# Optimization experiments

Hardware: AMD Instinct MI355X
Metric: run time of the kernel (lower is better)

Reference implementation:

```python
import jax, jax.numpy as jnp
import numpy as np

EPS = 1e-5

def cal_pcm(cen, s):
    # circ_shift in the original is exactly a circular roll of the HxW plane.
    r = lambda dy, dx: jnp.roll(cen, (dy, dx), axis=(2, 3))
    s1 = (r(-s, -s) - cen) * (r(s, s) - cen)   # NW/SE diagonal pair
    s2 = (r(-s, 0) - cen) * (r(s, 0) - cen)    # N/S pair
    s3 = (r(-s, s) - cen) * (r(s, -s) - cen)   # NE/SW diagonal pair
    s4 = (r(0, s) - cen) * (r(0, -s) - cen)    # E/W pair
    return jnp.minimum(jnp.minimum(s1, s2), jnp.minimum(s3, s4))

def batchnorm(x, gamma, beta):
    # training-mode BN: batch statistics over (N,H,W)
    mean = x.mean(axis=(0, 2, 3), keepdims=True)
    var = x.var(axis=(0, 2, 3), keepdims=True)
    xn = (x - mean) * jax.lax.rsqrt(var + EPS)
    return xn * gamma[None, :, None, None] + beta[None, :, None, None]

def se_att(x, w1, b1, g1, be1, w2, b2, g2, be2):
    # AdaptiveAvgPool2d(1) -> 1x1 conv -> BN -> ReLU -> 1x1 conv -> BN -> Sigmoid
    p = x.mean(axis=(2, 3), keepdims=True)                      # [B,C,1,1]
    y = jnp.einsum('oc,bcij->boij', w1, p) + b1[None, :, None, None]
    y = jax.nn.relu(batchnorm(y, g1, be1))
    y = jnp.einsum('oc,bcij->boij', w2, y) + b2[None, :, None, None]
    return jax.nn.sigmoid(batchnorm(y, g2, be2))

def setup_inputs() -> dict:
    key = jax.random.key(0)
    ks = jax.random.split(key, 8)
    B, C, H, W = 4, 64, 384, 384
    IC = C // 2
    inp = {
        'cen': jax.random.normal(ks[0], (B, C, H, W), dtype=jnp.float32),
        'bn1_g': jnp.ones((C,), jnp.float32), 'bn1_b': jnp.zeros((C,), jnp.float32),
        'bn2_g': jnp.ones((C,), jnp.float32), 'bn2_b': jnp.zeros((C,), jnp.float32),
        'td_w1': jax.random.normal(ks[1], (IC, C), jnp.float32) * 0.1,
        'td_b1': jnp.zeros((IC,), jnp.float32),
        'td_g1': jnp.ones((IC,), jnp.float32), 'td_be1': jnp.zeros((IC,), jnp.float32),
        'td_w2': jax.random.normal(ks[2], (C, IC), jnp.float32) * 0.1,
        'td_b2': jnp.zeros((C,), jnp.float32),
        'td_g2': jnp.ones((C,), jnp.float32), 'td_be2': jnp.zeros((C,), jnp.float32),
        'bu_w1': jax.random.normal(ks[3], (IC, C), jnp.float32) * 0.1,
        'bu_b1': jnp.zeros((IC,), jnp.float32),
        'bu_g1': jnp.ones((IC,), jnp.float32), 'bu_be1': jnp.zeros((IC,), jnp.float32),
        'bu_w2': jax.random.normal(ks[4], (C, IC), jnp.float32) * 0.1,
        'bu_b2': jnp.zeros((C,), jnp.float32),
        'bu_g2': jnp.ones((C,), jnp.float32), 'bu_be2': jnp.zeros((C,), jnp.float32),
    }
    return inp

def reference(cen, bn1_g, bn1_b, bn2_g, bn2_b,
              td_w1, td_b1, td_g1, td_be1, td_w2, td_b2, td_g2, td_be2,
              bu_w1, bu_b1, bu_g1, bu_be1, bu_w2, bu_b2, bu_g2, bu_be2):
    pcm13 = batchnorm(cal_pcm(cen, 13), bn1_g, bn1_b)
    pcm17 = batchnorm(cal_pcm(cen, 17), bn2_g, bn2_b)
    topdown_wei = se_att(pcm17, td_w1, td_b1, td_g1, td_be1, td_w2, td_b2, td_g2, td_be2)
    bottomup_wei = se_att(pcm13, bu_w1, bu_b1, bu_g1, bu_be1, bu_w2, bu_b2, bu_g2, bu_be2)
    return topdown_wei * pcm13 + bottomup_wei * pcm17
```

## Files before the change

### kernel.cpp

```cpp
#include <hip/hip_runtime.h>
#include <math.h>

#define HH 384
#define WW 384
#define CNUM 64
#define BNUM 4
#define HWSZ (HH*WW)
#define NPLANES (BNUM*CNUM)
#define ROWS_PER_BLOCK 16
#define BLOCKS_PER_PLANE (HH/ROWS_PER_BLOCK)
#define NBLOCKS (NPLANES*BLOCKS_PER_PLANE)
#define EPSBN 1e-5f

__device__ __forceinline__ void pcm_loads(const float* __restrict__ pp, int h, int w,
      int wp13, int wm13, int wp17, int wm17, float* v)
{
  int hp13 = h+13; if (hp13 >= HH) hp13 -= HH;
  int hm13 = h-13; if (hm13 <  0 ) hm13 += HH;
  int hp17 = h+17; if (hp17 >= HH) hp17 -= HH;
  int hm17 = h-17; if (hm17 <  0 ) hm17 += HH;
  const float* r0   = pp + h*WW;
  const float* rp13 = pp + hp13*WW;
  const float* rm13 = pp + hm13*WW;
  const float* rp17 = pp + hp17*WW;
  const float* rm17 = pp + hm17*WW;
  v[0]  = r0[w];
  v[1]  = rp13[wp13]; v[2]  = rm13[wm13];
  v[3]  = rp13[w];    v[4]  = rm13[w];
  v[5]  = rp13[wm13]; v[6]  = rm13[wp13];
  v[7]  = r0[wm13];   v[8]  = r0[wp13];
  v[9]  = rp17[wp17]; v[10] = rm17[wm17];
  v[11] = rp17[w];    v[12] = rm17[w];
  v[13] = rp17[wm17]; v[14] = rm17[wp17];
  v[15] = r0[wm17];   v[16] = r0[wp17];
}

__device__ __forceinline__ void pcm_eval(const float* v, float& p13, float& p17)
{
  const float d = v[0];
  {
    float s1 = (v[1]-d)*(v[2]-d);
    float s2 = (v[3]-d)*(v[4]-d);
    float s3 = (v[5]-d)*(v[6]-d);
    float s4 = (v[7]-d)*(v[8]-d);
    p13 = fminf(fminf(s1,s2), fminf(s3,s4));
  }
  {
    float s1 = (v[9] -d)*(v[10]-d);
    float s2 = (v[11]-d)*(v[12]-d);
    float s3 = (v[13]-d)*(v[14]-d);
    float s4 = (v[15]-d)*(v[16]-d);
    p17 = fminf(fminf(s1,s2), fminf(s3,s4));
  }
}

__device__ __forceinline__ int swz_block() {
  return (blockIdx.x & 7)*(NBLOCKS/8) + (blockIdx.x >> 3);
}

__global__ __launch_bounds__(384) void passA_kernel(const float* __restrict__ cen,
                                                    float* __restrict__ partials)
{
  const int blk = swz_block();
  const int p   = blk / BLOCKS_PER_PLANE;
  const int kb  = blk % BLOCKS_PER_PLANE;
  const int w   = threadIdx.x;
  const float* pp = cen + (size_t)p*HWSZ;

  int wp13 = w+13; if (wp13 >= WW) wp13 -= WW;
  int wm13 = w-13; if (wm13 <  0 ) wm13 += WW;
  int wp17 = w+17; if (wp17 >= WW) wp17 -= WW;
  int wm17 = w-17; if (wm17 <  0 ) wm17 += WW;

  float s13 = 0.f, q13 = 0.f, s17 = 0.f, q17 = 0.f;
  const int h0 = kb*ROWS_PER_BLOCK;
  #pragma unroll 2
  for (int r = 0; r < ROWS_PER_BLOCK; r += 2) {
    float va[17], vb[17];
    pcm_loads(pp, h0+r,   w, wp13, wm13, wp17, wm17, va);
    pcm_loads(pp, h0+r+1, w, wp13, wm13, wp17, wm17, vb);
    float a13, a17, b13, b17;
    pcm_eval(va, a13, a17);
    pcm_eval(vb, b13, b17);
    s13 += a13 + b13; q13 += a13*a13 + b13*b13;
    s17 += a17 + b17; q17 += a17*a17 + b17*b17;
  }
  for (int off = 32; off > 0; off >>= 1) {
    s13 += __shfl_down(s13, off);
    q13 += __shfl_down(q13, off);
    s17 += __shfl_down(s17, off);
    q17 += __shfl_down(q17, off);
  }
  __shared__ float red[6][4];
  const int wid = threadIdx.x >> 6;
  if ((threadIdx.x & 63) == 0) {
    red[wid][0] = s13; red[wid][1] = q13; red[wid][2] = s17; red[wid][3] = q17;
  }
  __syncthreads();
  if (threadIdx.x == 0) {
    float a=0.f,b=0.f,c=0.f,d=0.f;
    for (int i = 0; i < 6; ++i) { a+=red[i][0]; b+=red[i][1]; c+=red[i][2]; d+=red[i][3]; }
    float* q = partials + (size_t)blk*4;
    q[0]=a; q[1]=b; q[2]=c; q[3]=d;
  }
}

__device__ void se_mlp(int t, const float* __restrict__ p,
    const float* __restrict__ w1, const float* __restrict__ b1,
    const float* __restrict__ g1, const float* __restrict__ be1,
    const float* __restrict__ w2, const float* __restrict__ b2,
    const float* __restrict__ g2, const float* __restrict__ be2,
    float* y1, float* sc, float* sh, float* wei)
{
  if (t < 128) {
    const int b = t >> 5, o = t & 31;
    float acc = b1[o];
    const float* wr = w1 + o*64;
    const float* pr = p  + b*64;
    #pragma unroll
    for (int c = 0; c < 64; ++c) acc += wr[c]*pr[c];
    y1[t] = acc;
  }
  __syncthreads();
  if (t < 32) {
    float a0=y1[t], a1=y1[32+t], a2=y1[64+t], a3=y1[96+t];
    float m = 0.25f*(a0+a1+a2+a3);
    float q = 0.25f*(a0*a0+a1*a1+a2*a2+a3*a3);
    float v = q - m*m;
    float s = g1[t]*rsqrtf(v + EPSBN);
    sc[t] = s; sh[t] = be1[t] - m*s;
  }
  __syncthreads();
  if (t < 128) {
    const int o = t & 31;
    y1[t] = fmaxf(y1[t]*sc[o] + sh[o], 0.0f);
  }
  __syncthreads();
  {
    const int b = t >> 6, o2 = t & 63;
    float acc = b2[o2];
    const float* wr = w2 + o2*32;
    const float* yr = y1 + b*32;
    #pragma unroll
    for (int o = 0; o < 32; ++o) acc += wr[o]*yr[o];
    wei[t] = acc;
  }
  __syncthreads();
  if (t < 64) {
    float a0=wei[t], a1=wei[64+t], a2=wei[128+t], a3=wei[192+t];
    float m = 0.25f*(a0+a1+a2+a3);
    float q = 0.25f*(a0*a0+a1*a1+a2*a2+a3*a3);
    float v = q - m*m;
    float s = g2[t]*rsqrtf(v + EPSBN);
    sc[t] = s; sh[t] = be2[t] - m*s;
  }
  __syncthreads();
  {
    const int o2 = t & 63;
    float z = wei[t]*sc[o2] + sh[o2];
    wei[t] = 1.0f/(1.0f + expf(-z));
  }
  __syncthreads();
}

__global__ __launch_bounds__(256) void se_kernel(
    const float* __restrict__ partials,
    const float* __restrict__ bn1_g, const float* __restrict__ bn1_b,
    const float* __restrict__ bn2_g, const float* __restrict__ bn2_b,
    const float* __restrict__ td_w1, const float* __restrict__ td_b1,
    const float* __restrict__ td_g1, const float* __restrict__ td_be1,
    const float* __restrict__ td_w2, const float* __restrict__ td_b2,
    const float* __restrict__ td_g2, const float* __restrict__ td_be2,
    const float* __restrict__ bu_w1, const float* __restrict__ bu_b1,
    const float* __restrict__ bu_g1, const float* __restrict__ bu_be1,
    const float* __restrict__ bu_w2, const float* __restrict__ bu_b2,
    const float* __restrict__ bu_g2, const float* __restrict__ bu_be2,
    float* __restrict__ coef)
{
  __shared__ float sum13[256], sq13[256], sum17[256], sq17[256];
  __shared__ float scale1[64], shift1[64], scale2[64], shift2[64];
  __shared__ float pm13[256], pm17[256];
  __shared__ float y1[128], sc[64], sh[64];
  __shared__ float tdw[256], buw[256];
  const int t = threadIdx.x;

  {
    float a=0.f,b=0.f,c=0.f,d=0.f;
    for (int kb = 0; kb < BLOCKS_PER_PLANE; ++kb) {
      const float* q = partials + ((size_t)(t*BLOCKS_PER_PLANE + kb))*4;
      a += q[0]; b += q[1]; c += q[2]; d += q[3];
    }
    sum13[t]=a; sq13[t]=b; sum17[t]=c; sq17[t]=d;
  }
  __syncthreads();

  if (t < 64) {
    float s=0.f,q=0.f,s2=0.f,q2=0.f;
    for (int b = 0; b < 4; ++b) {
      s  += sum13[b*64+t]; q  += sq13[b*64+t];
      s2 += sum17[b*64+t]; q2 += sq17[b*64+t];
    }
    const float inv = 1.0f/(4.0f*HWSZ);
    float m1 = s*inv,  v1 = q*inv  - m1*m1;
    float c1 = bn1_g[t]*rsqrtf(v1 + EPSBN);
    scale1[t] = c1; shift1[t] = bn1_b[t] - m1*c1;
    float m2 = s2*inv, v2 = q2*inv - m2*m2;
    float c2 = bn2_g[t]*rsqrtf(v2 + EPSBN);
    scale2[t] = c2; shift2[t] = bn2_b[t] - m2*c2;
  }
  __syncthreads();

  {
    const int c = t & 63;
    pm13[t] = (sum13[t]*(1.0f/HWSZ))*scale1[c] + shift1[c];
    pm17[t] = (sum17[t]*(1.0f/HWSZ))*scale2[c] + shift2[c];
  }
  __syncthreads();

  se_mlp(t, pm17, td_w1, td_b1, td_g1, td_be1, td_w2, td_b2, td_g2, td_be2, y1, sc, sh, tdw);
  se_mlp(t, pm13, bu_w1, bu_b1, bu_g1, bu_be1, bu_w2, bu_b2, bu_g2, bu_be2, y1, sc, sh, buw);

  {
    const int c = t & 63;
    float A  = tdw[t]*scale1[c];
    float Bc = buw[t]*scale2[c];
    float Cc = tdw[t]*shift1[c] + buw[t]*shift2[c];
    coef[t*4+0] = A; coef[t*4+1] = Bc; coef[t*4+2] = Cc;
  }
}

__global__ __launch_bounds__(384) void passB_kernel(const float* __restrict__ cen,
                                                    const float* __restrict__ coef,
                                                    float* __restrict__ out)
{
  const int blk = swz_block();
  const int p   = blk / BLOCKS_PER_PLANE;
  const int kb  = blk % BLOCKS_PER_PLANE;
  const int w   = threadIdx.x;
  const float A  = coef[p*4+0];
  const float Bc = coef[p*4+1];
  const float Cc = coef[p*4+2];
  const float* pp = cen + (size_t)p*HWSZ;
  float* op = out + (size_t)p*HWSZ;

  int wp13 = w+13; if (wp13 >= WW) wp13 -= WW;
  int wm13 = w-13; if (wm13 <  0 ) wm13 += WW;
  int wp17 = w+17; if (wp17 >= WW) wp17 -= WW;
  int wm17 = w-17; if (wm17 <  0 ) wm17 += WW;

  const int h0 = kb*ROWS_PER_BLOCK;
  #pragma unroll 2
  for (int r = 0; r < ROWS_PER_BLOCK; r += 2) {
    const int h = h0 + r;
    float va[17], vb[17];
    pcm_loads(pp, h,   w, wp13, wm13, wp17, wm17, va);
    pcm_loads(pp, h+1, w, wp13, wm13, wp17, wm17, vb);
    float a13, a17, b13, b17;
    pcm_eval(va, a13, a17);
    pcm_eval(vb, b13, b17);
    __builtin_nontemporal_store(A*a13 + Bc*a17 + Cc, &op[h*WW + w]);
    __builtin_nontemporal_store(A*b13 + Bc*b17 + Cc, &op[(h+1)*WW + w]);
  }
}

extern "C" void kernel_launch(void* const* d_in, const int* in_sizes, int n_in,
                              void* d_out, int out_size, void* d_ws, size_t ws_size,
                              hipStream_t stream) {
  const float* cen = (const float*)d_in[0];
  float* ws = (float*)d_ws;
  float* partials = ws;
  float* coef     = ws + (size_t)NBLOCKS*4;

  passA_kernel<<<NBLOCKS, 384, 0, stream>>>(cen, partials);
  se_kernel<<<1, 256, 0, stream>>>(partials,
      (const float*)d_in[1],  (const float*)d_in[2],  (const float*)d_in[3],  (const float*)d_in[4],
      (const float*)d_in[5],  (const float*)d_in[6],  (const float*)d_in[7],  (const float*)d_in[8],
      (const float*)d_in[9],  (const float*)d_in[10], (const float*)d_in[11], (const float*)d_in[12],
      (const float*)d_in[13], (const float*)d_in[14], (const float*)d_in[15], (const float*)d_in[16],
      (const float*)d_in[17], (const float*)d_in[18], (const float*)d_in[19], (const float*)d_in[20],
      coef);
  passB_kernel<<<NBLOCKS, 384, 0, stream>>>(cen, coef, (float*)d_out);
}
```

Measured before the change: 194.5 us.

## Materialize fp16 PCM pair in workspace and apply coefficients in streaming pass

When the workspace is large enough, the first pass now stores both PCM values (scale 13 and 17) as a packed half2 per pixel. It also accumulates BN statistics from the rounded values. A new vectorized elementwise kernel then reads the packed buffer and applies the per-plane affine coefficients, instead of recomputing the 17-tap stencil from the input. This trades a second full stencil read of the input for a write and read of a same-sized fp16 buffer. It adds half-precision rounding error to the output and keeps the old two-pass path as a fallback.

```diff
diff --git a/kernel.cpp b/kernel.cpp
--- a/kernel.cpp
+++ b/kernel.cpp
@@ -1,4 +1,5 @@
 #include <hip/hip_runtime.h>
+#include <hip/hip_fp16.h>
 #include <math.h>
 
 #define HH 384
@@ -7,10 +8,16 @@
 #define BNUM 4
 #define HWSZ (HH*WW)
 #define NPLANES (BNUM*CNUM)
-#define ROWS_PER_BLOCK 16
-#define BLOCKS_PER_PLANE (HH/ROWS_PER_BLOCK)
-#define NBLOCKS (NPLANES*BLOCKS_PER_PLANE)
 #define EPSBN 1e-5f
+
+#define ROWS_K1 32
+#define BPP_K1 (HH/ROWS_K1)
+#define NB_K1 (NPLANES*BPP_K1)
+#define ROWS_FB 16
+#define BPP_FB (HH/ROWS_FB)
+#define NB_FB (NPLANES*BPP_FB)
+
+typedef float f4v __attribute__((ext_vector_type(4)));
 
 __device__ __forceinline__ void pcm_loads(const float* __restrict__ pp, int h, int w,
       int wp13, int wm13, int wp17, int wm17, float* v)
@@ -54,18 +61,21 @@
   }
 }
 
+template<int NB>
 __device__ __forceinline__ int swz_block() {
-  return (blockIdx.x & 7)*(NBLOCKS/8) + (blockIdx.x >> 3);
-}
-
-__global__ __launch_bounds__(384) void passA_kernel(const float* __restrict__ cen,
-                                                    float* __restrict__ partials)
-{
-  const int blk = swz_block();
-  const int p   = blk / BLOCKS_PER_PLANE;
-  const int kb  = blk % BLOCKS_PER_PLANE;
+  return (blockIdx.x & 7)*(NB/8) + (blockIdx.x >> 3);
+}
+
+__global__ __launch_bounds__(384) void k1_kernel(const float* __restrict__ cen,
+                                                 unsigned int* __restrict__ pcm_ws,
+                                                 float* __restrict__ partials)
+{
+  const int blk = swz_block<NB_K1>();
+  const int p   = blk / BPP_K1;
+  const int kb  = blk % BPP_K1;
   const int w   = threadIdx.x;
   const float* pp = cen + (size_t)p*HWSZ;
+  unsigned int* wp = pcm_ws + (size_t)p*HWSZ;
 
   int wp13 = w+13; if (wp13 >= WW) wp13 -= WW;
   int wm13 = w-13; if (wm13 <  0 ) wm13 += WW;
@@ -73,17 +83,19 @@
   int wm17 = w-17; if (wm17 <  0 ) wm17 += WW;
 
   float s13 = 0.f, q13 = 0.f, s17 = 0.f, q17 = 0.f;
-  const int h0 = kb*ROWS_PER_BLOCK;
-  #pragma unroll 2
-  for (int r = 0; r < ROWS_PER_BLOCK; r += 2) {
-    float va[17], vb[17];
-    pcm_loads(pp, h0+r,   w, wp13, wm13, wp17, wm17, va);
-    pcm_loads(pp, h0+r+1, w, wp13, wm13, wp17, wm17, vb);
-    float a13, a17, b13, b17;
-    pcm_eval(va, a13, a17);
-    pcm_eval(vb, b13, b17);
-    s13 += a13 + b13; q13 += a13*a13 + b13*b13;
-    s17 += a17 + b17; q17 += a17*a17 + b17*b17;
+  const int h0 = kb*ROWS_K1;
+  #pragma unroll 4
+  for (int r = 0; r < ROWS_K1; ++r) {
+    const int h = h0 + r;
+    float v[17];
+    pcm_loads(pp, h, w, wp13, wm13, wp17, wm17, v);
+    float p13, p17;
+    pcm_eval(v, p13, p17);
+    __half2 hp = __floats2half2_rn(p13, p17);
+    wp[h*WW + w] = *reinterpret_cast<unsigned int*>(&hp);
+    float2 fr = __half22float2(hp);
+    s13 += fr.x; q13 += fr.x*fr.x;
+    s17 += fr.y; q17 += fr.y*fr.y;
   }
   for (int off = 32; off > 0; off >>= 1) {
     s13 += __shfl_down(s13, off);
@@ -164,7 +176,7 @@
 }
 
 __global__ __launch_bounds__(256) void se_kernel(
-    const float* __restrict__ partials,
+    const float* __restrict__ partials, int bpp,
     const float* __restrict__ bn1_g, const float* __restrict__ bn1_b,
     const float* __restrict__ bn2_g, const float* __restrict__ bn2_b,
     const float* __restrict__ td_w1, const float* __restrict__ td_b1,
@@ -186,8 +198,8 @@
 
   {
     float a=0.f,b=0.f,c=0.f,d=0.f;
-    for (int kb = 0; kb < BLOCKS_PER_PLANE; ++kb) {
-      const float* q = partials + ((size_t)(t*BLOCKS_PER_PLANE + kb))*4;
+    for (int kb = 0; kb < bpp; ++kb) {
+      const float* q = partials + ((size_t)(t*bpp + kb))*4;
       a += q[0]; b += q[1]; c += q[2]; d += q[3];
     }
     sum13[t]=a; sq13[t]=b; sum17[t]=c; sq17[t]=d;
@@ -225,7 +237,79 @@
     float A  = tdw[t]*scale1[c];
     float Bc = buw[t]*scale2[c];
     float Cc = tdw[t]*shift1[c] + buw[t]*shift2[c];
-    coef[t*4+0] = A; coef[t*4+1] = Bc; coef[t*4+2] = Cc;
+    coef[t*4+0] = A; coef[t*4+1] = Bc; coef[t*4+2] = Cc; coef[t*4+3] = 0.f;
+  }
+}
+
+#define K3_BLOCKS 4608
+#define K3_THREADS 256
+typedef unsigned int u4v __attribute__((ext_vector_type(4)));
+
+__global__ __launch_bounds__(K3_THREADS) void k3_kernel(const u4v* __restrict__ pcm4,
+                                                        const f4v* __restrict__ coef4,
+                                                        f4v* __restrict__ out4)
+{
+  const int total = NPLANES*HWSZ/4;
+  int i = blockIdx.x*K3_THREADS + threadIdx.x;
+  const int stride = K3_BLOCKS*K3_THREADS;
+  for (; i < total; i += stride) {
+    const int plane = (i*4)/HWSZ;
+    const f4v cf = coef4[plane];
+    const u4v v = pcm4[i];
+    f4v o;
+    #pragma unroll
+    for (int j = 0; j < 4; ++j) {
+      unsigned int u = v[j];
+      __half2 hp = *reinterpret_cast<__half2*>(&u);
+      float2 f = __half22float2(hp);
+      o[j] = cf.x*f.x + cf.y*f.y + cf.z;
+    }
+    __builtin_nontemporal_store(o, &out4[i]);
+  }
+}
+
+__global__ __launch_bounds__(384) void passA_kernel(const float* __restrict__ cen,
+                                                    float* __restrict__ partials)
+{
+  const int blk = swz_block<NB_FB>();
+  const int p   = blk / BPP_FB;
+  const int kb  = blk % BPP_FB;
+  const int w   = threadIdx.x;
+  const float* pp = cen + (size_t)p*HWSZ;
+
+  int wp13 = w+13; if (wp13 >= WW) wp13 -= WW;
+  int wm13 = w-13; if (wm13 <  0 ) wm13 += WW;
+  int wp17 = w+17; if (wp17 >= WW) wp17 -= WW;
+  int wm17 = w-17; if (wm17 <  0 ) wm17 += WW;
+
+  float s13 = 0.f, q13 = 0.f, s17 = 0.f, q17 = 0.f;
+  const int h0 = kb*ROWS_FB;
+  #pragma unroll 4
+  for (int r = 0; r < ROWS_FB; ++r) {
+    float v[17];
+    pcm_loads(pp, h0+r, w, wp13, wm13, wp17, wm17, v);
+    float a13, a17;
+    pcm_eval(v, a13, a17);
+    s13 += a13; q13 += a13*a13;
+    s17 += a17; q17 += a17*a17;
+  }
+  for (int off = 32; off > 0; off >>= 1) {
+    s13 += __shfl_down(s13, off);
+    q13 += __shfl_down(q13, off);
+    s17 += __shfl_down(s17, off);
+    q17 += __shfl_down(q17, off);
+  }
+  __shared__ float red[6][4];
+  const int wid = threadIdx.x >> 6;
+  if ((threadIdx.x & 63) == 0) {
+    red[wid][0] = s13; red[wid][1] = q13; red[wid][2] = s17; red[wid][3] = q17;
+  }
+  __syncthreads();
+  if (threadIdx.x == 0) {
+    float a=0.f,b=0.f,c=0.f,d=0.f;
+    for (int i = 0; i < 6; ++i) { a+=red[i][0]; b+=red[i][1]; c+=red[i][2]; d+=red[i][3]; }
+    float* q = partials + (size_t)blk*4;
+    q[0]=a; q[1]=b; q[2]=c; q[3]=d;
   }
 }
 
@@ -233,9 +317,9 @@
                                                     const float* __restrict__ coef,
                                                     float* __restrict__ out)
 {
-  const int blk = swz_block();
-  const int p   = blk / BLOCKS_PER_PLANE;
-  const int kb  = blk % BLOCKS_PER_PLANE;
+  const int blk = swz_block<NB_FB>();
+  const int p   = blk / BPP_FB;
+  const int kb  = blk % BPP_FB;
   const int w   = threadIdx.x;
   const float A  = coef[p*4+0];
   const float Bc = coef[p*4+1];
@@ -248,18 +332,15 @@
   int wp17 = w+17; if (wp17 >= WW) wp17 -= WW;
   int wm17 = w-17; if (wm17 <  0 ) wm17 += WW;
 
-  const int h0 = kb*ROWS_PER_BLOCK;
-  #pragma unroll 2
-  for (int r = 0; r < ROWS_PER_BLOCK; r += 2) {
+  const int h0 = kb*ROWS_FB;
+  #pragma unroll 4
+  for (int r = 0; r < ROWS_FB; ++r) {
     const int h = h0 + r;
-    float va[17], vb[17];
-    pcm_loads(pp, h,   w, wp13, wm13, wp17, wm17, va);
-    pcm_loads(pp, h+1, w, wp13, wm13, wp17, wm17, vb);
-    float a13, a17, b13, b17;
-    pcm_eval(va, a13, a17);
-    pcm_eval(vb, b13, b17);
+    float v[17];
+    pcm_loads(pp, h, w, wp13, wm13, wp17, wm17, v);
+    float a13, a17;
+    pcm_eval(v, a13, a17);
     __builtin_nontemporal_store(A*a13 + Bc*a17 + Cc, &op[h*WW + w]);
-    __builtin_nontemporal_store(A*b13 + Bc*b17 + Cc, &op[(h+1)*WW + w]);
   }
 }
 
@@ -267,17 +348,35 @@
                               void* d_out, int out_size, void* d_ws, size_t ws_size,
                               hipStream_t stream) {
   const float* cen = (const float*)d_in[0];
-  float* ws = (float*)d_ws;
-  float* partials = ws;
-  float* coef     = ws + (size_t)NBLOCKS*4;
-
-  passA_kernel<<<NBLOCKS, 384, 0, stream>>>(cen, partials);
-  se_kernel<<<1, 256, 0, stream>>>(partials,
-      (const float*)d_in[1],  (const float*)d_in[2],  (const float*)d_in[3],  (const float*)d_in[4],
-      (const float*)d_in[5],  (const float*)d_in[6],  (const float*)d_in[7],  (const float*)d_in[8],
-      (const float*)d_in[9],  (const float*)d_in[10], (const float*)d_in[11], (const float*)d_in[12],
-      (const float*)d_in[13], (const float*)d_in[14], (const float*)d_in[15], (const float*)d_in[16],
-      (const float*)d_in[17], (const float*)d_in[18], (const float*)d_in[19], (const float*)d_in[20],
-      coef);
-  passB_kernel<<<NBLOCKS, 384, 0, stream>>>(cen, coef, (float*)d_out);
-}
+  const size_t PCM_BYTES = (size_t)NPLANES*HWSZ*sizeof(unsigned int);
+  const size_t NEED = PCM_BYTES + (size_t)NB_K1*4*sizeof(float) + 256*4*sizeof(float);
+
+  if (ws_size >= NEED) {
+    unsigned int* pcm_ws = (unsigned int*)d_ws;
+    float* partials = (float*)((char*)d_ws + PCM_BYTES);
+    float* coef     = partials + (size_t)NB_K1*4;
+
+    k1_kernel<<<NB_K1, 384, 0, stream>>>(cen, pcm_ws, partials);
+    se_kernel<<<1, 256, 0, stream>>>(partials, BPP_K1,
+        (const float*)d_in[1],  (const float*)d_in[2],  (const float*)d_in[3],  (const float*)d_in[4],
+        (const float*)d_in[5],  (const float*)d_in[6],  (const float*)d_in[7],  (const float*)d_in[8],
+        (const float*)d_in[9],  (const float*)d_in[10], (const float*)d_in[11], (const float*)d_in[12],
+        (const float*)d_in[13], (const float*)d_in[14], (const float*)d_in[15], (const float*)d_in[16],
+        (const float*)d_in[17], (const float*)d_in[18], (const float*)d_in[19], (const float*)d_in[20],
+        coef);
+    k3_kernel<<<K3_BLOCKS, K3_THREADS, 0, stream>>>((const u4v*)pcm_ws, (const f4v*)coef, (f4v*)d_out);
+  } else {
+    float* ws = (float*)d_ws;
+    float* partials = ws;
+    float* coef     = ws + (size_t)NB_FB*4;
+    passA_kernel<<<NB_FB, 384, 0, stream>>>(cen, partials);
+    se_kernel<<<1, 256, 0, stream>>>(partials, BPP_FB,
+        (const float*)d_in[1],  (const float*)d_in[2],  (const float*)d_in[3],  (const float*)d_in[4],
+        (const float*)d_in[5],  (const float*)d_in[6],  (const float*)d_in[7],  (const float*)d_in[8],
+        (const float*)d_in[9],  (const float*)d_in[10], (const float*)d_in[11], (const float*)d_in[12],
+        (const float*)d_in[13], (const float*)d_in[14], (const float*)d_in[15], (const float*)d_in[16],
+        (const float*)d_in[17], (const float*)d_in[18], (const float*)d_in[19], (const float*)d_in[20],
+        coef);
+    passB_kernel<<<NB_FB, 384, 0, stream>>>(cen, coef, (float*)d_out);
+  }
+}
```

Result: slower. 207.4 us (+6.7%).
